# Kernel optimization log

Measured on AMD Instinct MI355X. Metric: run time of the kernel, lower is better.

## Reference

```python
import jax, jax.numpy as jnp
import numpy as np


def setup_inputs() -> dict:
    key = jax.random.key(0)
    ks = jax.random.split(key, 5)
    H = 512
    batch = 128
    enc_len = 100
    num_layers = 1
    s = 1.0 / np.sqrt(H)  # torch default U(-1/sqrt(H), 1/sqrt(H)); use same scale
    return {
        "encoder_outputs": jax.random.normal(ks[0], (num_layers, batch, enc_len, H), jnp.float32),
        "W_ih": jax.random.uniform(ks[1], (3 * H, H), jnp.float32, -s, s),
        "W_hh": jax.random.uniform(ks[2], (3 * H, H), jnp.float32, -s, s),
        "b_ih": jax.random.uniform(ks[3], (3 * H,), jnp.float32, -s, s),
        "b_hh": jax.random.uniform(ks[4], (3 * H,), jnp.float32, -s, s),
        "out_len": 1024,
    }


def reference(encoder_outputs, W_ih, W_hh, b_ih, b_hh, out_len):
    # encoder_outputs: (num_layers, batch, enc_len, H); hidden init = last enc step
    h0 = encoder_outputs[:, :, -1][0]          # (batch, H), num_layers == 1
    batch, H = h0.shape
    x0 = jnp.zeros((batch, H), h0.dtype)        # initInput: zeros(batch, 1, H)

    def gru_cell(x, h):
        gi = x @ W_ih.T + b_ih                  # (batch, 3H)
        gh = h @ W_hh.T + b_hh                  # (batch, 3H)
        i_r, i_z, i_n = jnp.split(gi, 3, axis=-1)
        h_r, h_z, h_n = jnp.split(gh, 3, axis=-1)
        r = jax.nn.sigmoid(i_r + h_r)
        z = jax.nn.sigmoid(i_z + h_z)
        n = jnp.tanh(i_n + r * h_n)
        return (1.0 - z) * n + z * h

    def step(carry, _):
        x, h = carry
        h_new = gru_cell(x, h)                  # GRU output at t == new hidden (1 layer)
        # original does input = output.detach(): no grad through the input chain
        return (jax.lax.stop_gradient(h_new), h_new), h_new

    _, outs = jax.lax.scan(step, (x0, h0), None, length=out_len)  # (out_len, batch, H)
    # torch.cat(output) along dim 0 of (batch, 1, H) chunks -> (out_len*batch, 1, H)
    return outs.reshape(out_len * batch, 1, H)
```

## Files before the change

kernel.cpp:

```cpp
#include <hip/hip_runtime.h>
#include <hip/hip_bf16.h>

#define H        512
#define BATCH    128
#define OUTLEN   1024
#define RROWS    16
#define CBCOLS   64
#define NBLOCK   64
#define NTH      512
#define LSTR     520
#define GSTR     68

typedef __attribute__((ext_vector_type(8))) short short8;
typedef __attribute__((ext_vector_type(4))) float floatx4;
typedef __attribute__((ext_vector_type(2))) float floatx2;

static __device__ __forceinline__ unsigned short f2bf(float f) {
    unsigned u = __builtin_bit_cast(unsigned, f);
    unsigned r = u + 0x7FFFu + ((u >> 16) & 1u);
    return (unsigned short)(r >> 16);
}
static __device__ __forceinline__ float sigm(float x) { return 1.f / (1.f + __expf(-x)); }
static __device__ __forceinline__ float tanhc(float x) {
    x = fminf(fmaxf(x, -15.f), 15.f);
    float e = __expf(-2.f * x);
    return (1.f - e) / (1.f + e);
}

__global__ void gru_init(const float* __restrict__ enc, int enc_len,
                         const float* __restrict__ W_hh,
                         const float* __restrict__ b_ih, const float* __restrict__ b_hh,
                         float* __restrict__ out, unsigned short* __restrict__ hbuf,
                         float* __restrict__ h1buf, int* __restrict__ flags) {
    __shared__ float h0[2][H];
    const int tid = threadIdx.x;
    const int b0 = blockIdx.x * 2;
    for (int i = tid; i < 2 * H; i += NTH) {
        int r = i >> 9, k = i & (H - 1);
        h0[r][k] = enc[((size_t)(b0 + r) * enc_len + (enc_len - 1)) * H + k];
    }
    __syncthreads();
    const int c = tid;
    const float4* wr = (const float4*)(W_hh + (size_t)(0 * H + c) * H);
    const float4* wz = (const float4*)(W_hh + (size_t)(1 * H + c) * H);
    const float4* wn = (const float4*)(W_hh + (size_t)(2 * H + c) * H);
    float dr0 = 0.f, dz0 = 0.f, dn0 = 0.f, dr1 = 0.f, dz1 = 0.f, dn1 = 0.f;
    #pragma unroll 4
    for (int k4 = 0; k4 < H / 4; ++k4) {
        float4 a = wr[k4], b = wz[k4], d = wn[k4];
        const float* p0 = &h0[0][k4 * 4];
        const float* p1 = &h0[1][k4 * 4];
        dr0 += a.x * p0[0] + a.y * p0[1] + a.z * p0[2] + a.w * p0[3];
        dz0 += b.x * p0[0] + b.y * p0[1] + b.z * p0[2] + b.w * p0[3];
        dn0 += d.x * p0[0] + d.y * p0[1] + d.z * p0[2] + d.w * p0[3];
        dr1 += a.x * p1[0] + a.y * p1[1] + a.z * p1[2] + a.w * p1[3];
        dz1 += b.x * p1[0] + b.y * p1[1] + b.z * p1[2] + b.w * p1[3];
        dn1 += d.x * p1[0] + d.y * p1[1] + d.z * p1[2] + d.w * p1[3];
    }
    const float bir = b_ih[c], biz = b_ih[H + c], bin = b_ih[2 * H + c];
    const float bhr = b_hh[c], bhz = b_hh[H + c], bhn = b_hh[2 * H + c];
    unsigned short* hb1 = hbuf + (size_t)BATCH * H;
    {
        float r0 = sigm(bir + dr0 + bhr);
        float z0 = sigm(biz + dz0 + bhz);
        float n0 = tanhc(bin + r0 * (dn0 + bhn));
        float h1 = (1.f - z0) * n0 + z0 * h0[0][c];
        out[(size_t)b0 * H + c] = h1;
        h1buf[(size_t)b0 * H + c] = h1;
        __hip_atomic_store(hb1 + (size_t)b0 * H + c, f2bf(h1),
                           __ATOMIC_RELAXED, __HIP_MEMORY_SCOPE_AGENT);
    }
    {
        float r1 = sigm(bir + dr1 + bhr);
        float z1 = sigm(biz + dz1 + bhz);
        float n1 = tanhc(bin + r1 * (dn1 + bhn));
        float h1 = (1.f - z1) * n1 + z1 * h0[1][c];
        out[(size_t)(b0 + 1) * H + c] = h1;
        h1buf[(size_t)(b0 + 1) * H + c] = h1;
        __hip_atomic_store(hb1 + (size_t)(b0 + 1) * H + c, f2bf(h1),
                           __ATOMIC_RELAXED, __HIP_MEMORY_SCOPE_AGENT);
    }
    if (blockIdx.x == 0 && tid < NBLOCK)
        __hip_atomic_store(flags + tid, 0, __ATOMIC_RELAXED, __HIP_MEMORY_SCOPE_AGENT);
}

__launch_bounds__(NTH, 1)
__global__ void gru_main(const float* __restrict__ enc, int enc_len,
                         const float* __restrict__ W_ih, const float* __restrict__ W_hh,
                         const float* __restrict__ b_ih, const float* __restrict__ b_hh,
                         float* __restrict__ out,
                         unsigned short* __restrict__ hbuf, const float* __restrict__ h1buf,
                         int* __restrict__ flags) {
    __shared__ __align__(16) short hs[RROWS * LSTR];
    __shared__ float gacc[4][RROWS * GSTR];
    __shared__ float bias[4][CBCOLS];

    const int group  = blockIdx.x & 7;
    const int colblk = blockIdx.x >> 3;
    const int row0   = group * RROWS;
    const int col0   = colblk * CBCOLS;
    const int tid    = threadIdx.x;
    const int wid    = tid >> 6;
    const int lane   = tid & 63;
    const int l15    = lane & 15;
    const int quad   = lane >> 4;
    const int mat    = wid >> 1;
    const int ct0    = (wid & 1) * 2;

    short8 wf0[16], wf1[16];
    #pragma unroll
    for (int tt = 0; tt < 2; ++tt) {
        const int gc = col0 + (ct0 + tt) * 16 + l15;
        const float* a;
        const float* b = nullptr;
        if      (mat == 0) { a = W_ih + (size_t)gc * H;           b = W_hh + (size_t)gc * H; }
        else if (mat == 1) { a = W_ih + (size_t)(H + gc) * H;     b = W_hh + (size_t)(H + gc) * H; }
        else if (mat == 2) { a = W_ih + (size_t)(2 * H + gc) * H; }
        else               { a = W_hh + (size_t)(2 * H + gc) * H; }
        a += quad * 8;
        if (b) b += quad * 8;
        #pragma unroll
        for (int kk = 0; kk < 16; ++kk) {
            short8 f;
            #pragma unroll
            for (int j = 0; j < 8; ++j) {
                float v = a[kk * 32 + j];
                if (b) v += b[kk * 32 + j];
                f[j] = (short)f2bf(v);
            }
            if (tt == 0) wf0[kk] = f; else wf1[kk] = f;
        }
    }
    if (tid < 4 * CBCOLS) {
        int m = tid >> 6, c = tid & 63, gc = col0 + c;
        float v;
        if      (m == 0) v = b_ih[gc] + b_hh[gc];
        else if (m == 1) v = b_ih[H + gc] + b_hh[H + gc];
        else if (m == 2) v = b_ih[2 * H + gc];
        else             v = b_hh[2 * H + gc];
        bias[m][c] = v;
    }
    const int er = tid >> 5, ep = tid & 31;
    float st0, st1;
    {
        const float* p = h1buf + (size_t)(row0 + er) * H + col0 + 2 * ep;
        st0 = p[0];
        st1 = p[1];
    }
    __syncthreads();

    const unsigned long long* hb64 = (const unsigned long long*)hbuf;
    unsigned int* hb32 = (unsigned int*)hbuf;

    for (int t = 1; t < OUTLEN; ++t) {
        if (t > 1 && lane < 8) {
            int* fp = flags + lane * 8 + group;
            while (__hip_atomic_load(fp, __ATOMIC_RELAXED, __HIP_MEMORY_SCOPE_AGENT) < t) { }
        }
        {
            const unsigned long long* sp = hb64 + (size_t)(t & 1) * 16384 + (size_t)row0 * 128;
            unsigned long long vv[4];
            #pragma unroll
            for (int j = 0; j < 4; ++j)
                vv[j] = __hip_atomic_load(sp + j * NTH + tid,
                                          __ATOMIC_RELAXED, __HIP_MEMORY_SCOPE_AGENT);
            #pragma unroll
            for (int j = 0; j < 4; ++j) {
                int p = j * NTH + tid;
                *reinterpret_cast<unsigned long long*>(hs + (p >> 7) * LSTR + (p & 127) * 4) = vv[j];
            }
        }
        __syncthreads();

        floatx4 acc00 = {0.f,0.f,0.f,0.f}, acc01 = {0.f,0.f,0.f,0.f};
        floatx4 acc10 = {0.f,0.f,0.f,0.f}, acc11 = {0.f,0.f,0.f,0.f};
        {
            const short* arow = hs + l15 * LSTR + quad * 8;
            #pragma unroll
            for (int kk = 0; kk < 16; kk += 2) {
                short8 a0 = *reinterpret_cast<const short8*>(arow + kk * 32);
                short8 a1 = *reinterpret_cast<const short8*>(arow + (kk + 1) * 32);
                acc00 = __builtin_amdgcn_mfma_f32_16x16x32_bf16(a0, wf0[kk],     acc00, 0, 0, 0);
                acc10 = __builtin_amdgcn_mfma_f32_16x16x32_bf16(a0, wf1[kk],     acc10, 0, 0, 0);
                acc01 = __builtin_amdgcn_mfma_f32_16x16x32_bf16(a1, wf0[kk + 1], acc01, 0, 0, 0);
                acc11 = __builtin_amdgcn_mfma_f32_16x16x32_bf16(a1, wf1[kk + 1], acc11, 0, 0, 0);
            }
        }
        #pragma unroll
        for (int i = 0; i < 4; ++i) {
            gacc[mat][(quad * 4 + i) * GSTR + ct0 * 16 + l15]       = acc00[i] + acc01[i];
            gacc[mat][(quad * 4 + i) * GSTR + (ct0 + 1) * 16 + l15] = acc10[i] + acc11[i];
        }
        __syncthreads();

        {
            const int i0 = er * GSTR + 2 * ep, c = 2 * ep;
            float rr0 = sigm(gacc[0][i0]     + bias[0][c]);
            float rr1 = sigm(gacc[0][i0 + 1] + bias[0][c + 1]);
            float zz0 = sigm(gacc[1][i0]     + bias[1][c]);
            float zz1 = sigm(gacc[1][i0 + 1] + bias[1][c + 1]);
            float nn0 = tanhc(gacc[2][i0]     + bias[2][c]     + rr0 * (gacc[3][i0]     + bias[3][c]));
            float nn1 = tanhc(gacc[2][i0 + 1] + bias[2][c + 1] + rr1 * (gacc[3][i0 + 1] + bias[3][c + 1]));
            st0 = (1.f - zz0) * nn0 + zz0 * st0;
            st1 = (1.f - zz1) * nn1 + zz1 * st1;
            unsigned val = (unsigned)f2bf(st0) | ((unsigned)f2bf(st1) << 16);
            __hip_atomic_store(hb32 + (size_t)((t + 1) & 1) * 32768
                                    + (size_t)(row0 + er) * 256 + (col0 >> 1) + ep,
                               val, __ATOMIC_RELAXED, __HIP_MEMORY_SCOPE_AGENT);
        }
        __syncthreads();
        if (tid == 0)
            __hip_atomic_store(flags + blockIdx.x, t + 1,
                               __ATOMIC_RELAXED, __HIP_MEMORY_SCOPE_AGENT);
        {
            floatx2 o = {st0, st1};
            *reinterpret_cast<floatx2*>(out + ((size_t)t * BATCH + row0 + er) * H + col0 + 2 * ep) = o;
        }
    }
}

extern "C" void kernel_launch(void* const* d_in, const int* in_sizes, int n_in,
                              void* d_out, int out_size, void* d_ws, size_t ws_size,
                              hipStream_t stream) {
    const float* enc  = (const float*)d_in[0];
    const float* W_ih = (const float*)d_in[1];
    const float* W_hh = (const float*)d_in[2];
    const float* b_ih = (const float*)d_in[3];
    const float* b_hh = (const float*)d_in[4];
    float* out = (float*)d_out;
    int enc_len = in_sizes[0] / (BATCH * H);

    unsigned short* hbuf = (unsigned short*)d_ws;
    int* flags = (int*)((char*)d_ws + (size_t)2 * BATCH * H * sizeof(unsigned short));
    float* h1buf = (float*)((char*)flags + 256);

    hipLaunchKernelGGL(gru_init, dim3(NBLOCK), dim3(NTH), 0, stream,
                       enc, enc_len, W_hh, b_ih, b_hh, out, hbuf, h1buf, flags);

    void* args[] = { (void*)&enc, (void*)&enc_len, (void*)&W_ih, (void*)&W_hh,
                     (void*)&b_ih, (void*)&b_hh, (void*)&out, (void*)&hbuf,
                     (void*)&h1buf, (void*)&flags };
    hipError_t err = hipLaunchCooperativeKernel((const void*)gru_main, dim3(NBLOCK),
                                                dim3(NTH), args, 0, stream);
    if (err != hipSuccess) {
        hipLaunchKernelGGL(gru_main, dim3(NBLOCK), dim3(NTH), 0, stream,
                           enc, enc_len, W_ih, W_hh, b_ih, b_hh, out, hbuf, h1buf, flags);
    }
}
```

Baseline: 2.804 ms.

## Pad per-block flags and let each wave wait only on its own producer

Each flag now sits on its own padded slot (stride of 32 ints), so the pollers no longer share a cache line with the flags being written. Each wave's lane 0 now spins only on the flag of the single producer block whose hidden-state columns that wave loads, then copies just that producer's slice into LDS. The previous scheme had every wave wait on all eight producers. The h1 staging buffer is dropped and the initial state is read back from the output instead. The aim is lower cross-block synchronisation latency per timestep, since waves can begin loading as soon as their own producer is ready, at the cost of an uncoalesced, per-wave load pattern.

```diff
diff --git a/kernel.cpp b/kernel.cpp
--- a/kernel.cpp
+++ b/kernel.cpp
@@ -10,6 +10,7 @@
 #define NTH      512
 #define LSTR     520
 #define GSTR     68
+#define FSTR     32
 
 typedef __attribute__((ext_vector_type(8))) short short8;
 typedef __attribute__((ext_vector_type(4))) float floatx4;
@@ -31,7 +32,7 @@
                          const float* __restrict__ W_hh,
                          const float* __restrict__ b_ih, const float* __restrict__ b_hh,
                          float* __restrict__ out, unsigned short* __restrict__ hbuf,
-                         float* __restrict__ h1buf, int* __restrict__ flags) {
+                         int* __restrict__ flags) {
     __shared__ float h0[2][H];
     const int tid = threadIdx.x;
     const int b0 = blockIdx.x * 2;
@@ -66,7 +67,6 @@
         float n0 = tanhc(bin + r0 * (dn0 + bhn));
         float h1 = (1.f - z0) * n0 + z0 * h0[0][c];
         out[(size_t)b0 * H + c] = h1;
-        h1buf[(size_t)b0 * H + c] = h1;
         __hip_atomic_store(hb1 + (size_t)b0 * H + c, f2bf(h1),
                            __ATOMIC_RELAXED, __HIP_MEMORY_SCOPE_AGENT);
     }
@@ -76,12 +76,12 @@
         float n1 = tanhc(bin + r1 * (dn1 + bhn));
         float h1 = (1.f - z1) * n1 + z1 * h0[1][c];
         out[(size_t)(b0 + 1) * H + c] = h1;
-        h1buf[(size_t)(b0 + 1) * H + c] = h1;
         __hip_atomic_store(hb1 + (size_t)(b0 + 1) * H + c, f2bf(h1),
                            __ATOMIC_RELAXED, __HIP_MEMORY_SCOPE_AGENT);
     }
     if (blockIdx.x == 0 && tid < NBLOCK)
-        __hip_atomic_store(flags + tid, 0, __ATOMIC_RELAXED, __HIP_MEMORY_SCOPE_AGENT);
+        __hip_atomic_store(flags + tid * FSTR, 0,
+                           __ATOMIC_RELAXED, __HIP_MEMORY_SCOPE_AGENT);
 }
 
 __launch_bounds__(NTH, 1)
@@ -89,8 +89,7 @@
                          const float* __restrict__ W_ih, const float* __restrict__ W_hh,
                          const float* __restrict__ b_ih, const float* __restrict__ b_hh,
                          float* __restrict__ out,
-                         unsigned short* __restrict__ hbuf, const float* __restrict__ h1buf,
-                         int* __restrict__ flags) {
+                         unsigned short* __restrict__ hbuf, int* __restrict__ flags) {
     __shared__ __align__(16) short hs[RROWS * LSTR];
     __shared__ float gacc[4][RROWS * GSTR];
     __shared__ float bias[4][CBCOLS];
@@ -143,7 +142,7 @@
     const int er = tid >> 5, ep = tid & 31;
     float st0, st1;
     {
-        const float* p = h1buf + (size_t)(row0 + er) * H + col0 + 2 * ep;
+        const float* p = out + (size_t)(row0 + er) * H + col0 + 2 * ep;
         st0 = p[0];
         st1 = p[1];
     }
@@ -153,21 +152,26 @@
     unsigned int* hb32 = (unsigned int*)hbuf;
 
     for (int t = 1; t < OUTLEN; ++t) {
-        if (t > 1 && lane < 8) {
-            int* fp = flags + lane * 8 + group;
-            while (__hip_atomic_load(fp, __ATOMIC_RELAXED, __HIP_MEMORY_SCOPE_AGENT) < t) { }
-        }
-        {
-            const unsigned long long* sp = hb64 + (size_t)(t & 1) * 16384 + (size_t)row0 * 128;
+        if (t > 1 && lane == 0) {
+            const int* fp = flags + (wid * 8 + group) * FSTR;
+            while (__hip_atomic_load(fp, __ATOMIC_RELAXED,
+                                     __HIP_MEMORY_SCOPE_AGENT) < t) { }
+        }
+        {
+            const unsigned long long* sp = hb64 + (size_t)(t & 1) * 16384
+                                                + (size_t)row0 * 128 + wid * 16;
             unsigned long long vv[4];
             #pragma unroll
-            for (int j = 0; j < 4; ++j)
-                vv[j] = __hip_atomic_load(sp + j * NTH + tid,
+            for (int j = 0; j < 4; ++j) {
+                int i = j * 64 + lane;
+                vv[j] = __hip_atomic_load(sp + (i >> 4) * 128 + (i & 15),
                                           __ATOMIC_RELAXED, __HIP_MEMORY_SCOPE_AGENT);
+            }
             #pragma unroll
             for (int j = 0; j < 4; ++j) {
-                int p = j * NTH + tid;
-                *reinterpret_cast<unsigned long long*>(hs + (p >> 7) * LSTR + (p & 127) * 4) = vv[j];
+                int i = j * 64 + lane;
+                *reinterpret_cast<unsigned long long*>(
+                    hs + (i >> 4) * LSTR + (wid * 16 + (i & 15)) * 4) = vv[j];
             }
         }
         __syncthreads();
@@ -210,7 +214,7 @@
         }
         __syncthreads();
         if (tid == 0)
-            __hip_atomic_store(flags + blockIdx.x, t + 1,
+            __hip_atomic_store(flags + blockIdx.x * FSTR, t + 1,
                                __ATOMIC_RELAXED, __HIP_MEMORY_SCOPE_AGENT);
         {
             floatx2 o = {st0, st1};
@@ -232,18 +236,17 @@
 
     unsigned short* hbuf = (unsigned short*)d_ws;
     int* flags = (int*)((char*)d_ws + (size_t)2 * BATCH * H * sizeof(unsigned short));
-    float* h1buf = (float*)((char*)flags + 256);
 
     hipLaunchKernelGGL(gru_init, dim3(NBLOCK), dim3(NTH), 0, stream,
-                       enc, enc_len, W_hh, b_ih, b_hh, out, hbuf, h1buf, flags);
+                       enc, enc_len, W_hh, b_ih, b_hh, out, hbuf, flags);
 
     void* args[] = { (void*)&enc, (void*)&enc_len, (void*)&W_ih, (void*)&W_hh,
                      (void*)&b_ih, (void*)&b_hh, (void*)&out, (void*)&hbuf,
-                     (void*)&h1buf, (void*)&flags };
+                     (void*)&flags };
     hipError_t err = hipLaunchCooperativeKernel((const void*)gru_main, dim3(NBLOCK),
                                                 dim3(NTH), args, 0, stream);
     if (err != hipSuccess) {
         hipLaunchKernelGGL(gru_main, dim3(NBLOCK), dim3(NTH), 0, stream,
-                           enc, enc_len, W_ih, W_hh, b_ih, b_hh, out, hbuf, h1buf, flags);
-    }
-}
+                           enc, enc_len, W_ih, W_hh, b_ih, b_hh, out, hbuf, flags);
+    }
+}
```

After: 2.605 ms. -7.1%, faster.

## Replace flag-based inter-block sync with step-tagged hidden-state words

Applied to the files above, without the earlier changes.

Each bf16 pair of hidden state is now stored as a 64-bit word whose upper half carries a magic value plus the timestep. Consumers poll the data directly until every word carries the expected tag, which removes the separate flag array, the extra __syncthreads and the flag store per step. The initial state is read from the output buffer instead of a separate fp32 copy. Each data load is twice as wide, and spinning on data means repeated reloads of the full tile. Stale tags from a previous launch could match only if the magic value and step happened to collide.

```diff
diff --git a/kernel.cpp b/kernel.cpp
--- a/kernel.cpp
+++ b/kernel.cpp
@@ -10,6 +10,7 @@
 #define NTH      512
 #define LSTR     520
 #define GSTR     68
+#define TMAGIC   0x5AD00000u
 
 typedef __attribute__((ext_vector_type(8))) short short8;
 typedef __attribute__((ext_vector_type(4))) float floatx4;
@@ -27,12 +28,13 @@
     return (1.f - e) / (1.f + e);
 }
 
+
 __global__ void gru_init(const float* __restrict__ enc, int enc_len,
                          const float* __restrict__ W_hh,
                          const float* __restrict__ b_ih, const float* __restrict__ b_hh,
-                         float* __restrict__ out, unsigned short* __restrict__ hbuf,
-                         float* __restrict__ h1buf, int* __restrict__ flags) {
+                         float* __restrict__ out, unsigned long long* __restrict__ hbuf) {
     __shared__ float h0[2][H];
+    __shared__ float h1s[2][H];
     const int tid = threadIdx.x;
     const int b0 = blockIdx.x * 2;
     for (int i = tid; i < 2 * H; i += NTH) {
@@ -59,16 +61,13 @@
     }
     const float bir = b_ih[c], biz = b_ih[H + c], bin = b_ih[2 * H + c];
     const float bhr = b_hh[c], bhz = b_hh[H + c], bhn = b_hh[2 * H + c];
-    unsigned short* hb1 = hbuf + (size_t)BATCH * H;
     {
         float r0 = sigm(bir + dr0 + bhr);
         float z0 = sigm(biz + dz0 + bhz);
         float n0 = tanhc(bin + r0 * (dn0 + bhn));
         float h1 = (1.f - z0) * n0 + z0 * h0[0][c];
         out[(size_t)b0 * H + c] = h1;
-        h1buf[(size_t)b0 * H + c] = h1;
-        __hip_atomic_store(hb1 + (size_t)b0 * H + c, f2bf(h1),
-                           __ATOMIC_RELAXED, __HIP_MEMORY_SCOPE_AGENT);
+        h1s[0][c] = h1;
     }
     {
         float r1 = sigm(bir + dr1 + bhr);
@@ -76,21 +75,26 @@
         float n1 = tanhc(bin + r1 * (dn1 + bhn));
         float h1 = (1.f - z1) * n1 + z1 * h0[1][c];
         out[(size_t)(b0 + 1) * H + c] = h1;
-        h1buf[(size_t)(b0 + 1) * H + c] = h1;
-        __hip_atomic_store(hb1 + (size_t)(b0 + 1) * H + c, f2bf(h1),
+        h1s[1][c] = h1;
+    }
+    __syncthreads();
+    {
+        int r = tid >> 8;
+        int p = tid & 255;
+        unsigned v = (unsigned)f2bf(h1s[r][2 * p])
+                   | ((unsigned)f2bf(h1s[r][2 * p + 1]) << 16);
+        unsigned long long atom =
+            ((unsigned long long)(TMAGIC + 1u) << 32) | v;
+        __hip_atomic_store(hbuf + (size_t)32768 + (size_t)(b0 + r) * 256 + p, atom,
                            __ATOMIC_RELAXED, __HIP_MEMORY_SCOPE_AGENT);
     }
-    if (blockIdx.x == 0 && tid < NBLOCK)
-        __hip_atomic_store(flags + tid, 0, __ATOMIC_RELAXED, __HIP_MEMORY_SCOPE_AGENT);
 }
 
 __launch_bounds__(NTH, 1)
 __global__ void gru_main(const float* __restrict__ enc, int enc_len,
                          const float* __restrict__ W_ih, const float* __restrict__ W_hh,
                          const float* __restrict__ b_ih, const float* __restrict__ b_hh,
-                         float* __restrict__ out,
-                         unsigned short* __restrict__ hbuf, const float* __restrict__ h1buf,
-                         int* __restrict__ flags) {
+                         float* __restrict__ out, unsigned long long* __restrict__ hbuf) {
     __shared__ __align__(16) short hs[RROWS * LSTR];
     __shared__ float gacc[4][RROWS * GSTR];
     __shared__ float bias[4][CBCOLS];
@@ -143,32 +147,37 @@
     const int er = tid >> 5, ep = tid & 31;
     float st0, st1;
     {
-        const float* p = h1buf + (size_t)(row0 + er) * H + col0 + 2 * ep;
+        const float* p = out + (size_t)(row0 + er) * H + col0 + 2 * ep;
         st0 = p[0];
         st1 = p[1];
     }
     __syncthreads();
 
-    const unsigned long long* hb64 = (const unsigned long long*)hbuf;
-    unsigned int* hb32 = (unsigned int*)hbuf;
+    const int q  = lane & 31;
+    const int rb = lane >> 5;
 
     for (int t = 1; t < OUTLEN; ++t) {
-        if (t > 1 && lane < 8) {
-            int* fp = flags + lane * 8 + group;
-            while (__hip_atomic_load(fp, __ATOMIC_RELAXED, __HIP_MEMORY_SCOPE_AGENT) < t) { }
-        }
-        {
-            const unsigned long long* sp = hb64 + (size_t)(t & 1) * 16384 + (size_t)row0 * 128;
-            unsigned long long vv[4];
+        {
+            const unsigned long long* sp = hbuf + (size_t)(t & 1) * 32768
+                                                + (size_t)(row0 + rb) * 256
+                                                + (size_t)wid * 32 + q;
+            const unsigned etag = TMAGIC + (unsigned)t;
+            unsigned long long vv[8];
+            for (;;) {
+                #pragma unroll
+                for (int j = 0; j < 8; ++j)
+                    vv[j] = __hip_atomic_load(sp + (size_t)(512 * j),
+                                              __ATOMIC_RELAXED, __HIP_MEMORY_SCOPE_AGENT);
+                bool ok = true;
+                #pragma unroll
+                for (int j = 0; j < 8; ++j)
+                    ok &= ((unsigned)(vv[j] >> 32) == etag);
+                if (__all(ok)) break;
+            }
             #pragma unroll
-            for (int j = 0; j < 4; ++j)
-                vv[j] = __hip_atomic_load(sp + j * NTH + tid,
-                                          __ATOMIC_RELAXED, __HIP_MEMORY_SCOPE_AGENT);
-            #pragma unroll
-            for (int j = 0; j < 4; ++j) {
-                int p = j * NTH + tid;
-                *reinterpret_cast<unsigned long long*>(hs + (p >> 7) * LSTR + (p & 127) * 4) = vv[j];
-            }
+            for (int j = 0; j < 8; ++j)
+                *reinterpret_cast<unsigned*>(hs + (rb + 2 * j) * LSTR + wid * 64 + 2 * q)
+                    = (unsigned)vv[j];
         }
         __syncthreads();
 
@@ -204,14 +213,12 @@
             st0 = (1.f - zz0) * nn0 + zz0 * st0;
             st1 = (1.f - zz1) * nn1 + zz1 * st1;
             unsigned val = (unsigned)f2bf(st0) | ((unsigned)f2bf(st1) << 16);
-            __hip_atomic_store(hb32 + (size_t)((t + 1) & 1) * 32768
-                                    + (size_t)(row0 + er) * 256 + (col0 >> 1) + ep,
-                               val, __ATOMIC_RELAXED, __HIP_MEMORY_SCOPE_AGENT);
-        }
-        __syncthreads();
-        if (tid == 0)
-            __hip_atomic_store(flags + blockIdx.x, t + 1,
-                               __ATOMIC_RELAXED, __HIP_MEMORY_SCOPE_AGENT);
+            unsigned long long atom =
+                ((unsigned long long)(TMAGIC + (unsigned)(t + 1)) << 32) | val;
+            __hip_atomic_store(hbuf + (size_t)((t + 1) & 1) * 32768
+                                    + (size_t)(row0 + er) * 256 + colblk * 32 + ep,
+                               atom, __ATOMIC_RELAXED, __HIP_MEMORY_SCOPE_AGENT);
+        }
         {
             floatx2 o = {st0, st1};
             *reinterpret_cast<floatx2*>(out + ((size_t)t * BATCH + row0 + er) * H + col0 + 2 * ep) = o;
@@ -230,20 +237,17 @@
     float* out = (float*)d_out;
     int enc_len = in_sizes[0] / (BATCH * H);
 
-    unsigned short* hbuf = (unsigned short*)d_ws;
-    int* flags = (int*)((char*)d_ws + (size_t)2 * BATCH * H * sizeof(unsigned short));
-    float* h1buf = (float*)((char*)flags + 256);
+    unsigned long long* hbuf = (unsigned long long*)d_ws;
 
     hipLaunchKernelGGL(gru_init, dim3(NBLOCK), dim3(NTH), 0, stream,
-                       enc, enc_len, W_hh, b_ih, b_hh, out, hbuf, h1buf, flags);
+                       enc, enc_len, W_hh, b_ih, b_hh, out, hbuf);
 
     void* args[] = { (void*)&enc, (void*)&enc_len, (void*)&W_ih, (void*)&W_hh,
-                     (void*)&b_ih, (void*)&b_hh, (void*)&out, (void*)&hbuf,
-                     (void*)&h1buf, (void*)&flags };
+                     (void*)&b_ih, (void*)&b_hh, (void*)&out, (void*)&hbuf };
     hipError_t err = hipLaunchCooperativeKernel((const void*)gru_main, dim3(NBLOCK),
                                                 dim3(NTH), args, 0, stream);
     if (err != hipSuccess) {
         hipLaunchKernelGGL(gru_main, dim3(NBLOCK), dim3(NTH), 0, stream,
-                           enc, enc_len, W_ih, W_hh, b_ih, b_hh, out, hbuf, h1buf, flags);
-    }
-}
+                           enc, enc_len, W_ih, W_hh, b_ih, b_hh, out, hbuf);
+    }
+}
```

After: 3.042 ms. 8.5% more time.
